# Kernel tuning notes

Hardware: AMD Instinct MI355X
Metric: run time of the kernel (lower is better)

## Reference

```python
import jax, jax.numpy as jnp
import numpy as np

KS = 63          # kernel_size
SIGMA = 32.0     # sigma


def setup_inputs() -> dict:
    key = jax.random.key(0)
    k1, k2, k3 = jax.random.split(key, 3)
    B, C, H, W = 8, 31, 512, 512
    x = jax.random.normal(k1, (B, C, H, W), dtype=jnp.float32)
    dx_noise = jax.random.normal(k2, (B, 1, H, W), dtype=jnp.float32)
    dy_noise = jax.random.normal(k3, (B, 1, H, W), dtype=jnp.float32)
    return {"x": x, "dx_noise": dx_noise, "dy_noise": dy_noise}


def _blur(d):
    # reflect-pad by KS//2 then 'valid' conv with the (one-sided, unnormalized)
    # Gaussian outer-product kernel exp(-i^2/(2*sigma^2)) -- matches torch exactly.
    # The 2D kernel is rank-1, so apply it as two 1D passes (same math).
    pad = KS // 2
    k1d = jnp.exp(-(jnp.arange(KS, dtype=jnp.float32) ** 2) / (2.0 * SIGMA ** 2))
    dp = jnp.pad(d, ((0, 0), (0, 0), (pad, pad), (pad, pad)), mode='reflect')
    kv = k1d.reshape(1, 1, KS, 1)
    kh = k1d.reshape(1, 1, 1, KS)
    dn = jax.lax.conv_general_dilated(dp, kv, (1, 1), 'VALID',
                                      dimension_numbers=('NCHW', 'OIHW', 'NCHW'))
    dn = jax.lax.conv_general_dilated(dn, kh, (1, 1), 'VALID',
                                      dimension_numbers=('NCHW', 'OIHW', 'NCHW'))
    return dn  # [B,1,H,W]


def _grid_sample_bilinear_border(x, grid):
    # x: [B,C,H,W], grid: [B,H,W,2] in [-1,1], align_corners=True, border padding
    B, C, H, W = x.shape
    ix = (grid[..., 0] + 1.0) * 0.5 * (W - 1)
    iy = (grid[..., 1] + 1.0) * 0.5 * (H - 1)
    ix = jnp.clip(ix, 0.0, W - 1)  # border padding: clamp coords
    iy = jnp.clip(iy, 0.0, H - 1)
    x0 = jnp.floor(ix)
    y0 = jnp.floor(iy)
    wx = ix - x0  # [B,H,W]
    wy = iy - y0
    x0i = x0.astype(jnp.int32)
    y0i = y0.astype(jnp.int32)
    x1i = jnp.clip(x0i + 1, 0, W - 1)
    y1i = jnp.clip(y0i + 1, 0, H - 1)

    def per_image(img, y0i, y1i, x0i, x1i, wx, wy):
        # img: [C,H,W]; index maps: [H,W]
        v00 = img[:, y0i, x0i]
        v01 = img[:, y0i, x1i]
        v10 = img[:, y1i, x0i]
        v11 = img[:, y1i, x1i]
        return (v00 * (1 - wx) * (1 - wy) + v01 * wx * (1 - wy)
                + v10 * (1 - wx) * wy + v11 * wx * wy)

    return jax.vmap(per_image)(x, y0i, y1i, x0i, x1i, wx, wy)


def reference(x, dx_noise, dy_noise):
    B, C, H, W = x.shape
    dx = _blur(dx_noise)
    dy = _blur(dy_noise)
    # global (whole-tensor, cross-batch) max normalization, as in torch
    dx = dx * SIGMA / jnp.max(dx)
    dy = dy * SIGMA / jnp.max(dy)
    gy, gx = jnp.meshgrid(jnp.arange(H, dtype=jnp.float32),
                          jnp.arange(W, dtype=jnp.float32), indexing='ij')
    base = jnp.stack([gx, gy], axis=-1)                       # [H,W,2] (x,y)
    disp = jnp.concatenate([dx, dy], axis=1).transpose(0, 2, 3, 1)  # [B,H,W,2]
    grid = base[None] + disp
    grid = 2.0 * grid / jnp.array([W - 1, H - 1], dtype=jnp.float32) - 1.0
    warped = _grid_sample_bilinear_border(x, grid)
    return warped, grid
```

## Files before the change

### kernel.cpp

```cpp
#include <hip/hip_runtime.h>
#include <math.h>

#define SIGMA_F 32.0f
#define BB 8
#define CC 31
#define HH 512
#define WW 512
#define PLANE (HH * WW)

constexpr double cexp_neg(double t) {
    double u = -t / 16.0;
    double s = 1.0, term = 1.0;
    for (int k = 1; k < 14; ++k) { term *= u / (double)k; s += term; }
    s = s * s; s = s * s; s = s * s; s = s * s;
    return s;
}
constexpr float gwf(int i) { return (float)cexp_neg((double)(i * i) / 2048.0); }

__device__ constexpr float W[64] = {
    gwf(0),  gwf(1),  gwf(2),  gwf(3),  gwf(4),  gwf(5),  gwf(6),  gwf(7),
    gwf(8),  gwf(9),  gwf(10), gwf(11), gwf(12), gwf(13), gwf(14), gwf(15),
    gwf(16), gwf(17), gwf(18), gwf(19), gwf(20), gwf(21), gwf(22), gwf(23),
    gwf(24), gwf(25), gwf(26), gwf(27), gwf(28), gwf(29), gwf(30), gwf(31),
    gwf(32), gwf(33), gwf(34), gwf(35), gwf(36), gwf(37), gwf(38), gwf(39),
    gwf(40), gwf(41), gwf(42), gwf(43), gwf(44), gwf(45), gwf(46), gwf(47),
    gwf(48), gwf(49), gwf(50), gwf(51), gwf(52), gwf(53), gwf(54), gwf(55),
    gwf(56), gwf(57), gwf(58), gwf(59), gwf(60), gwf(61), gwf(62), 0.0f
};

__global__ __launch_bounds__(256, 2) void blur_fused_kernel(const float* __restrict__ dxn,
                                                            const float* __restrict__ dyn,
                                                            float* __restrict__ blur,
                                                            float* __restrict__ partials) {
    __shared__ __align__(16) float vt[16 * 580];
    __shared__ float smax[4];
    int t = threadIdx.x;
    int blk = blockIdx.x;
    int plane = blk >> 5;
    int band = blk & 31;
    int y0 = band << 4;
    const float* src = (plane < BB) ? dxn + (size_t)plane * PLANE
                                    : dyn + (size_t)(plane - BB) * PLANE;

    for (int c = t; c < 574; c += 256) {
        int L = c - 31;
        int scol = (L < 0) ? -L : ((L > HH - 1) ? 2 * HH - 2 - L : L);
        float acc[16];
        #pragma unroll
        for (int j = 0; j < 16; ++j) acc[j] = 0.0f;
        #pragma unroll
        for (int ro = 0; ro < 78; ++ro) {
            int rr = y0 - 31 + ro;
            int r = (rr < 0) ? -rr : ((rr > HH - 1) ? 2 * HH - 2 - rr : rr);
            float v = src[r * WW + scol];
            #pragma unroll
            for (int j = 0; j < 16; ++j) {
                int wi = ro - j;
                if (wi >= 0 && wi < 63) acc[j] += W[wi] * v;
            }
        }
        #pragma unroll
        for (int j = 0; j < 16; ++j) vt[j * 580 + c] = acc[j];
    }
    __syncthreads();

    float m = -INFINITY;
    int row = t & 15;
    int chunk0 = t >> 4;
    float* dstrow = blur + (size_t)plane * PLANE + (size_t)(y0 + row) * WW;
    const float* vrow = vt + row * 580;
    #pragma unroll
    for (int pass = 0; pass < 2; ++pass) {
        int x0 = (chunk0 + (pass << 4)) << 4;
        float acc[16];
        #pragma unroll
        for (int j = 0; j < 16; ++j) acc[j] = 0.0f;
        const float4* v4 = (const float4*)(vrow + x0);
        #pragma unroll
        for (int mi = 0; mi < 20; ++mi) {
            float4 vv = v4[mi];
            #pragma unroll
            for (int e = 0; e < 4; ++e) {
                float xv = (e == 0) ? vv.x : (e == 1) ? vv.y : (e == 2) ? vv.z : vv.w;
                int k = (mi << 2) + e;
                #pragma unroll
                for (int j = 0; j < 16; ++j) {
                    int wi = k - j;
                    if (wi >= 0 && wi < 63) acc[j] += W[wi] * xv;
                }
            }
        }
        #pragma unroll
        for (int j = 0; j < 16; ++j) m = fmaxf(m, acc[j]);
        float4* dst4 = (float4*)(dstrow + x0);
        #pragma unroll
        for (int q = 0; q < 4; ++q)
            dst4[q] = make_float4(acc[4 * q], acc[4 * q + 1], acc[4 * q + 2], acc[4 * q + 3]);
    }

    for (int off = 32; off; off >>= 1) m = fmaxf(m, __shfl_down(m, off, 64));
    if ((t & 63) == 0) smax[t >> 6] = m;
    __syncthreads();
    if (t == 0)
        partials[blk] = fmaxf(fmaxf(smax[0], smax[1]), fmaxf(smax[2], smax[3]));
}

__global__ __launch_bounds__(256) void reduce_max_kernel(const float* __restrict__ partials,
                                                         float* __restrict__ maxv) {
    int f = blockIdx.x;
    int t = threadIdx.x;
    float m = partials[f * 256 + t];
    __shared__ float smax[4];
    for (int off = 32; off; off >>= 1) m = fmaxf(m, __shfl_down(m, off, 64));
    if ((t & 63) == 0) smax[t >> 6] = m;
    __syncthreads();
    if (t == 0)
        maxv[f] = fmaxf(fmaxf(smax[0], smax[1]), fmaxf(smax[2], smax[3]));
}

__device__ __forceinline__ void gload_lds16(const float* g, float* l) {
    __builtin_amdgcn_global_load_lds(
        (const __attribute__((address_space(1))) void*)g,
        (__attribute__((address_space(3))) void*)l,
        16, 0, 0);
}

__global__ __launch_bounds__(256) void warp_tiled_kernel(const float* __restrict__ xin,
                                                         const float* __restrict__ blur,
                                                         const float* __restrict__ maxv,
                                                         float* __restrict__ warped,
                                                         float2* __restrict__ gridout) {
    __shared__ __align__(16) float stage[128 * 128];
    __shared__ int rx0[4], rx1[4], ry0[4], ry1[4];
    __shared__ int sokv;

    int t = threadIdx.x;
    int bid = blockIdx.x;
    int b = bid & 7;
    int tile = bid >> 3;
    int ty0 = (tile >> 3) << 6;
    int tx0 = (tile & 7) << 6;
    int wxs = min(max(tx0 - 32, 0), WW - 128);
    int wys = min(max(ty0 - 32, 0), HH - 128);

    float sx = SIGMA_F / maxv[0];
    float sy = SIGMA_F / maxv[1];
    int col = t & 63, row0 = t >> 6;

    float wxa[16], wya[16];
    int oa[16];
    int x0mn = 1 << 30, x0mx = -1, y0mn = 1 << 30, y0mx = -1;

    const float* bdx = blur + (size_t)b * PLANE;
    const float* bdy = blur + (size_t)(BB + b) * PLANE;

    #pragma unroll
    for (int k = 0; k < 16; ++k) {
        int gy = ty0 + row0 + 4 * k;
        int gx = tx0 + col;
        float dxv = bdx[gy * WW + gx] * sx;
        float dyv = bdy[gy * WW + gx] * sy;
        float gnx = 2.0f * ((float)gx + dxv) / 511.0f - 1.0f;
        float gny = 2.0f * ((float)gy + dyv) / 511.0f - 1.0f;
        gridout[((size_t)b * HH + gy) * WW + gx] = make_float2(gnx, gny);
        float ix = (gnx + 1.0f) * 0.5f * 511.0f;
        float iy = (gny + 1.0f) * 0.5f * 511.0f;
        ix = fminf(fmaxf(ix, 0.0f), 511.0f);
        iy = fminf(fmaxf(iy, 0.0f), 511.0f);
        float fx = floorf(ix), fy = floorf(iy);
        float wx = ix - fx, wy = iy - fy;
        int x0 = (int)fx, y0 = (int)fy;
        if (x0 > WW - 2) { x0 = WW - 2; wx = 1.0f; }
        if (y0 > HH - 2) { y0 = HH - 2; wy = 1.0f; }
        wxa[k] = wx; wya[k] = wy;
        oa[k] = (y0 - wys) * 128 + (x0 - wxs);
        x0mn = min(x0mn, x0); x0mx = max(x0mx, x0);
        y0mn = min(y0mn, y0); y0mx = max(y0mx, y0);
    }

    for (int off = 32; off; off >>= 1) {
        x0mn = min(x0mn, __shfl_xor(x0mn, off, 64));
        x0mx = max(x0mx, __shfl_xor(x0mx, off, 64));
        y0mn = min(y0mn, __shfl_xor(y0mn, off, 64));
        y0mx = max(y0mx, __shfl_xor(y0mx, off, 64));
    }
    if ((t & 63) == 0) {
        int wv = t >> 6;
        rx0[wv] = x0mn; rx1[wv] = x0mx; ry0[wv] = y0mn; ry1[wv] = y0mx;
    }
    __syncthreads();
    if (t == 0) {
        int a = rx0[0], bx = rx1[0], c = ry0[0], d = ry1[0];
        #pragma unroll
        for (int i = 1; i < 4; ++i) {
            a = min(a, rx0[i]); bx = max(bx, rx1[i]);
            c = min(c, ry0[i]); d = max(d, ry1[i]);
        }
        sokv = (a >= wxs) && (bx <= wxs + 126) && (c >= wys) && (d <= wys + 126);
    }
    __syncthreads();
    int ok = sokv;

    const float* xb = xin + (size_t)b * CC * PLANE;
    float* wb = warped + (size_t)b * CC * PLANE;
    int obase = (ty0 + row0) * WW + tx0 + col;

    if (ok) {
        int wave = t >> 6, lane = t & 63;
        int srow = 2 * wave + (lane >> 5);
        int scol4 = (lane & 31) * 4;
        const float* gbase = xb + (size_t)(wys + srow) * WW + wxs + scol4;
        float* lbase = stage + 2 * wave * 128;

        for (int c = 0; c < CC; ++c) {
            const float* g = gbase + (size_t)c * PLANE;
            #pragma unroll
            for (int i = 0; i < 16; ++i)
                gload_lds16(g + i * 8 * WW, lbase + i * 8 * 128);
            __syncthreads();
            float* dstc = wb + (size_t)c * PLANE;
            #pragma unroll
            for (int k = 0; k < 16; ++k) {
                float v00 = stage[oa[k]],       v01 = stage[oa[k] + 1];
                float v10 = stage[oa[k] + 128], v11 = stage[oa[k] + 129];
                float tp = v00 + wxa[k] * (v01 - v00);
                float bt = v10 + wxa[k] * (v11 - v10);
                dstc[obase + k * 4 * WW] = tp + wya[k] * (bt - tp);
            }
            __syncthreads();
        }
    } else {
        #pragma unroll
        for (int k = 0; k < 16; ++k) {
            int gy = ty0 + row0 + 4 * k;
            int gx = tx0 + col;
            float dxv = bdx[gy * WW + gx] * sx;
            float dyv = bdy[gy * WW + gx] * sy;
            float gnx = 2.0f * ((float)gx + dxv) / 511.0f - 1.0f;
            float gny = 2.0f * ((float)gy + dyv) / 511.0f - 1.0f;
            float ix = (gnx + 1.0f) * 0.5f * 511.0f;
            float iy = (gny + 1.0f) * 0.5f * 511.0f;
            ix = fminf(fmaxf(ix, 0.0f), 511.0f);
            iy = fminf(fmaxf(iy, 0.0f), 511.0f);
            float fx = floorf(ix), fy = floorf(iy);
            float wx = ix - fx, wy = iy - fy;
            int x0 = (int)fx, y0 = (int)fy;
            if (x0 > WW - 2) { x0 = WW - 2; wx = 1.0f; }
            if (y0 > HH - 2) { y0 = HH - 2; wy = 1.0f; }
            int o00 = y0 * WW + x0;
            for (int c = 0; c < CC; ++c) {
                const float* src = xb + (size_t)c * PLANE;
                float v00 = src[o00], v01 = src[o00 + 1];
                float v10 = src[o00 + WW], v11 = src[o00 + WW + 1];
                float tp = v00 + wx * (v01 - v00);
                float bt = v10 + wx * (v11 - v10);
                wb[(size_t)c * PLANE + obase + k * 4 * WW] = tp + wy * (bt - tp);
            }
        }
    }
}

extern "C" void kernel_launch(void* const* d_in, const int* in_sizes, int n_in,
                              void* d_out, int out_size, void* d_ws, size_t ws_size,
                              hipStream_t stream) {
    const float* x   = (const float*)d_in[0];
    const float* dxn = (const float*)d_in[1];
    const float* dyn = (const float*)d_in[2];

    float* ws = (float*)d_ws;
    float* blur     = ws;
    float* partials = ws + 4194304;
    float* maxv     = ws + 4194304 + 512;

    float* warped   = (float*)d_out;
    float2* gridout = (float2*)((float*)d_out + (size_t)BB * CC * PLANE);

    blur_fused_kernel<<<16 * 32, 256, 0, stream>>>(dxn, dyn, blur, partials);
    reduce_max_kernel<<<2, 256, 0, stream>>>(partials, maxv);
    warp_tiled_kernel<<<BB * 64, 256, 0, stream>>>(x, blur, maxv, warped, gridout);
}
```

Baseline: 162.3 us.

## Double-buffer LDS channel staging with prefetch and 512-thread blocks

The warp kernel now allocates two 128x128 LDS staging buffers. While the current channel is being interpolated, it issues the async global-to-LDS loads for the next channel, using explicit vmcnt waits and raw s_barrier calls in place of the full __syncthreads pairs. The block size doubles to 512 threads, so each thread handles 8 output rows instead of 16. The goal is to hide global load latency behind interpolation and stores. The cost is 128KB of LDS per block, which limits occupancy to about one block per CU. Because CDNA counts stores in vmcnt, the vmcnt waits also wait on earlier stores.

Result: slower. 199.3 us (+22.8%).

```diff
diff --git a/kernel.cpp b/kernel.cpp
--- a/kernel.cpp
+++ b/kernel.cpp
@@ -7,6 +7,7 @@
 #define HH 512
 #define WW 512
 #define PLANE (HH * WW)
+#define WINF (128 * 128)
 
 constexpr double cexp_neg(double t) {
     double u = -t / 16.0;
@@ -125,13 +126,13 @@
         16, 0, 0);
 }
 
-__global__ __launch_bounds__(256) void warp_tiled_kernel(const float* __restrict__ xin,
+__global__ __launch_bounds__(512) void warp_tiled_kernel(const float* __restrict__ xin,
                                                          const float* __restrict__ blur,
                                                          const float* __restrict__ maxv,
                                                          float* __restrict__ warped,
                                                          float2* __restrict__ gridout) {
-    __shared__ __align__(16) float stage[128 * 128];
-    __shared__ int rx0[4], rx1[4], ry0[4], ry1[4];
+    __shared__ __align__(16) float stage[2 * WINF];
+    __shared__ int rx0[8], rx1[8], ry0[8], ry1[8];
     __shared__ int sokv;
 
     int t = threadIdx.x;
@@ -147,16 +148,16 @@
     float sy = SIGMA_F / maxv[1];
     int col = t & 63, row0 = t >> 6;
 
-    float wxa[16], wya[16];
-    int oa[16];
+    float wxa[8], wya[8];
+    int oa[8];
     int x0mn = 1 << 30, x0mx = -1, y0mn = 1 << 30, y0mx = -1;
 
     const float* bdx = blur + (size_t)b * PLANE;
     const float* bdy = blur + (size_t)(BB + b) * PLANE;
 
     #pragma unroll
-    for (int k = 0; k < 16; ++k) {
-        int gy = ty0 + row0 + 4 * k;
+    for (int k = 0; k < 8; ++k) {
+        int gy = ty0 + row0 + 8 * k;
         int gx = tx0 + col;
         float dxv = bdx[gy * WW + gx] * sx;
         float dyv = bdy[gy * WW + gx] * sy;
@@ -192,7 +193,7 @@
     if (t == 0) {
         int a = rx0[0], bx = rx1[0], c = ry0[0], d = ry1[0];
         #pragma unroll
-        for (int i = 1; i < 4; ++i) {
+        for (int i = 1; i < 8; ++i) {
             a = min(a, rx0[i]); bx = max(bx, rx1[i]);
             c = min(c, ry0[i]); d = max(d, ry1[i]);
         }
@@ -210,29 +211,46 @@
         int srow = 2 * wave + (lane >> 5);
         int scol4 = (lane & 31) * 4;
         const float* gbase = xb + (size_t)(wys + srow) * WW + wxs + scol4;
-        float* lbase = stage + 2 * wave * 128;
+        int lofs = srow * 128;
+
+        #pragma unroll
+        for (int i = 0; i < 8; ++i)
+            gload_lds16(gbase + i * 16 * WW, stage + lofs + i * 16 * 128);
 
         for (int c = 0; c < CC; ++c) {
-            const float* g = gbase + (size_t)c * PLANE;
-            #pragma unroll
-            for (int i = 0; i < 16; ++i)
-                gload_lds16(g + i * 8 * WW, lbase + i * 8 * 128);
-            __syncthreads();
+            int cur = c & 1;
+            if (c < CC - 1) {
+                const float* g = gbase + (size_t)(c + 1) * PLANE;
+                float* l = stage + (cur ^ 1) * WINF + lofs;
+                #pragma unroll
+                for (int i = 0; i < 8; ++i)
+                    gload_lds16(g + i * 16 * WW, l + i * 16 * 128);
+                asm volatile("s_waitcnt vmcnt(8)" ::: "memory");
+            } else {
+                asm volatile("s_waitcnt vmcnt(0)" ::: "memory");
+            }
+            __builtin_amdgcn_sched_barrier(0);
+            __builtin_amdgcn_s_barrier();
+            __builtin_amdgcn_sched_barrier(0);
+
+            const float* sb = stage + cur * WINF;
             float* dstc = wb + (size_t)c * PLANE;
             #pragma unroll
-            for (int k = 0; k < 16; ++k) {
-                float v00 = stage[oa[k]],       v01 = stage[oa[k] + 1];
-                float v10 = stage[oa[k] + 128], v11 = stage[oa[k] + 129];
+            for (int k = 0; k < 8; ++k) {
+                float v00 = sb[oa[k]],       v01 = sb[oa[k] + 1];
+                float v10 = sb[oa[k] + 128], v11 = sb[oa[k] + 129];
                 float tp = v00 + wxa[k] * (v01 - v00);
                 float bt = v10 + wxa[k] * (v11 - v10);
-                dstc[obase + k * 4 * WW] = tp + wya[k] * (bt - tp);
-            }
-            __syncthreads();
+                dstc[obase + k * 8 * WW] = tp + wya[k] * (bt - tp);
+            }
+            __builtin_amdgcn_sched_barrier(0);
+            __builtin_amdgcn_s_barrier();
+            __builtin_amdgcn_sched_barrier(0);
         }
     } else {
         #pragma unroll
-        for (int k = 0; k < 16; ++k) {
-            int gy = ty0 + row0 + 4 * k;
+        for (int k = 0; k < 8; ++k) {
+            int gy = ty0 + row0 + 8 * k;
             int gx = tx0 + col;
             float dxv = bdx[gy * WW + gx] * sx;
             float dyv = bdy[gy * WW + gx] * sy;
@@ -254,7 +272,7 @@
                 float v10 = src[o00 + WW], v11 = src[o00 + WW + 1];
                 float tp = v00 + wx * (v01 - v00);
                 float bt = v10 + wx * (v11 - v10);
-                wb[(size_t)c * PLANE + obase + k * 4 * WW] = tp + wy * (bt - tp);
+                wb[(size_t)c * PLANE + obase + k * 8 * WW] = tp + wy * (bt - tp);
             }
         }
     }
@@ -277,5 +295,5 @@
 
     blur_fused_kernel<<<16 * 32, 256, 0, stream>>>(dxn, dyn, blur, partials);
     reduce_max_kernel<<<2, 256, 0, stream>>>(partials, maxv);
-    warp_tiled_kernel<<<BB * 64, 256, 0, stream>>>(x, blur, maxv, warped, gridout);
-}
+    warp_tiled_kernel<<<BB * 64, 512, 0, stream>>>(x, blur, maxv, warped, gridout);
+}
```
